# Kernel optimization log

Hardware: AMD Instinct MI355X
Metric: run time of the kernel (lower is better)

The kernel has to match this reference:

```python
import jax, jax.numpy as jnp
import numpy as np

B, L, D, DH = 4, 2048, 1024, 2048

def setup_inputs() -> dict:
    key = jax.random.key(0)
    ks = jax.random.split(key, 9)
    return {
        "x": jax.random.normal(ks[0], (B, L, D), jnp.float32),
        "W_in": jax.random.normal(ks[1], (DH, D), jnp.float32) / np.sqrt(D).astype(np.float32),
        "b_in": jnp.zeros((DH,), jnp.float32),
        "W_out": jax.random.normal(ks[2], (D, DH), jnp.float32) / np.sqrt(DH).astype(np.float32),
        "b_out": jnp.zeros((D,), jnp.float32),
        "phazor": jax.random.normal(ks[3], (DH, 2), jnp.float32),
        "phazor_init": jax.random.normal(ks[4], (DH, 2), jnp.float32),
        "last_conv_re": jax.random.normal(ks[5], (B, DH), jnp.float32),
        "last_conv_im": jax.random.normal(ks[6], (B, DH), jnp.float32),
    }

def reference(x, W_in, b_in, W_out, b_out, phazor, phazor_init, last_conv_re, last_conv_im):
    batch, length, _ = x.shape
    # linear_in, cast to float32 (already fp32 here)
    h = x @ W_in.T + b_in                                  # [B, L, DH]
    # view_as_complex of [DH, 2] params
    p = phazor[:, 0] + 1j * phazor[:, 1]                   # [DH]
    p0 = phazor_init[:, 0] + 1j * phazor_init[:, 1]        # [DH]
    pa = jnp.abs(p)
    p = p / pa * jnp.exp(-pa)                              # unit phase, exp(-|p|) magnitude
    # phazor_progression[t, c] = p[c] ** t
    prog = p[None, :] ** jnp.arange(length)[:, None]       # [L, DH] complex
    filt = prog * p0[None, :]                              # [L, DH]
    # FFT convolution with zero padding to 2L (linear convolution)
    ff = jnp.fft.fft(filt, n=2 * length, axis=0)           # [2L, DH]
    xf = jnp.fft.fft(h, n=2 * length, axis=1)              # [B, 2L, DH]
    conv = jnp.fft.ifft(ff[None] * xf, axis=1)[:, :length] # [B, L, DH]
    # add decayed contribution of past state (detached state)
    last = last_conv_re + 1j * last_conv_im                # [B, DH]
    conv_with_past = conv + last[:, None, :] * prog[None] * p[None, None, :]
    y = jax.nn.silu(conv_with_past.real)                   # back to real dtype
    return y @ W_out.T + b_out                             # [B, L, D]
```

## Files before the change

kernel.cpp:

```cpp
#include <hip/hip_runtime.h>
#include <math.h>

#define WS_B  4
#define WS_L  2048
#define WS_D  1024
#define WS_DH 2048
#define WS_M  (WS_B * WS_L)
#define NCH   128
#define CHUNK (WS_L / NCH)
#define CB    8

typedef __attribute__((ext_vector_type(4))) float     f32x4;
typedef _Float16 f16x8 __attribute__((ext_vector_type(8)));
typedef _Float16 f16x4 __attribute__((ext_vector_type(4)));

#define GLDS(gptr, lptr) \
    __builtin_amdgcn_global_load_lds( \
        (const __attribute__((address_space(1))) unsigned int*)(gptr), \
        (__attribute__((address_space(3))) unsigned int*)(lptr), 16, 0, 0)

__device__ inline void pack_tile(const float* __restrict__ src, _Float16* __restrict__ dst,
                                 int K, int rb, int kb, int tid, _Float16 (*sT)[136]) {
    const int K8 = K >> 3;
#pragma unroll
    for (int it = 0; it < 16; ++it) {
        int f    = it * 256 + tid;
        int row  = f >> 5;
        int col  = (f & 31) * 4;
        f32x4 v  = *(const f32x4*)(src + (size_t)(rb * 128 + row) * K + kb * 128 + col);
        f16x4 hv;
#pragma unroll
        for (int k = 0; k < 4; ++k) hv[k] = (_Float16)v[k];
        *(f16x4*)&sT[row][col] = hv;
    }
    __syncthreads();
#pragma unroll
    for (int it = 0; it < 8; ++it) {
        int c2 = it * 256 + tid;
        int r  = c2 & 127;
        int kq = c2 >> 7;
        f16x8 hv = *(const f16x8*)&sT[r][kq * 8];
        size_t chunk = ((size_t)rb * K8 + kb * 16 + kq) * 128 + r;
        *(f16x8*)(dst + chunk * 8) = hv;
    }
}

__global__ __launch_bounds__(256)
void pack_all(const float* __restrict__ x,     _Float16* __restrict__ xp,
              const float* __restrict__ W_in,  _Float16* __restrict__ w1p,
              const float* __restrict__ W_out, _Float16* __restrict__ w2p) {
    __shared__ alignas(16) _Float16 sT[128][136];
    const int tid = threadIdx.x;
    const int bid = blockIdx.x;
    if (bid < 512)      pack_tile(x,     xp,  WS_D,  bid >> 3,          bid & 7,          tid, sT);
    else if (bid < 640) pack_tile(W_in,  w1p, WS_D,  (bid - 512) >> 3,  (bid - 512) & 7,  tid, sT);
    else                pack_tile(W_out, w2p, WS_DH, (bid - 640) >> 4,  (bid - 640) & 15, tid, sT);
}

template<int K8, int LDC, int KQ, int MINB, typename OutT>
__global__ __launch_bounds__(256, MINB)
void gemm_f16_packed(const _Float16* __restrict__ A, const _Float16* __restrict__ B,
                     const float* __restrict__ bias, OutT* __restrict__ C)
{
    __shared__ alignas(16) _Float16 sA[2][KQ][128][8];
    __shared__ alignas(16) _Float16 sB[2][KQ][128][8];

    const int tid  = threadIdx.x;
    const int lane = tid & 63;
    const int wave = tid >> 6;
    const int wm   = (wave >> 1) * 64;
    const int wn   = (wave & 1) * 64;
    const int m15  = lane & 15;
    const int q    = lane >> 4;

    const int bm = blockIdx.x;
    const int bn = blockIdx.y;

    f32x4 acc[4][4] = {};

    auto stage = [&](int kc0, int buf) {
#pragma unroll
        for (int i = 0; i < KQ / 2; ++i) {
            int c   = i * 256 + tid;
            int row = c & 127;
            int kq  = c >> 7;
            size_t ac = ((size_t)(bm * K8 + kc0 + kq) * 128 + row) * 8;
            size_t bc = ((size_t)(bn * K8 + kc0 + kq) * 128 + row) * 8;
            GLDS(A + ac, &sA[buf][kq][row][0]);
            GLDS(B + bc, &sB[buf][kq][row][0]);
        }
    };

    auto compute = [&](int bufc) {
#pragma unroll
        for (int kk = 0; kk < KQ / 4; ++kk) {
            f16x8 af[4], bf[4];
#pragma unroll
            for (int i = 0; i < 4; ++i) {
                af[i] = *(const f16x8*)&sA[bufc][kk * 4 + q][wm + i * 16 + m15][0];
                bf[i] = *(const f16x8*)&sB[bufc][kk * 4 + q][wn + i * 16 + m15][0];
            }
#pragma unroll
            for (int i = 0; i < 4; ++i)
#pragma unroll
                for (int j = 0; j < 4; ++j)
                    acc[i][j] = __builtin_amdgcn_mfma_f32_16x16x32_f16(af[i], bf[j], acc[i][j], 0, 0, 0);
        }
    };

    stage(0, 0);
    stage(KQ, 1);

    int buf = 0;
    for (int kc0 = 0; kc0 + KQ < K8; kc0 += KQ, buf ^= 1) {
        asm volatile("s_waitcnt vmcnt(8)" ::: "memory");
        __builtin_amdgcn_sched_barrier(0);
        __builtin_amdgcn_s_barrier();

        compute(buf);

        __builtin_amdgcn_sched_barrier(0);
        __builtin_amdgcn_s_barrier();
        if (kc0 + 2 * KQ < K8) stage(kc0 + 2 * KQ, buf);
    }

    asm volatile("s_waitcnt vmcnt(0)" ::: "memory");
    __builtin_amdgcn_sched_barrier(0);
    __builtin_amdgcn_s_barrier();
    compute(buf);

    const int r4 = (lane >> 4) * 4;
#pragma unroll
    for (int j = 0; j < 4; ++j) {
        int col = bn * 128 + wn + j * 16 + m15;
        float bv = bias[col];
#pragma unroll
        for (int i = 0; i < 4; ++i) {
            int row0 = bm * 128 + wm + i * 16 + r4;
#pragma unroll
            for (int r = 0; r < 4; ++r)
                C[(size_t)(row0 + r) * LDC + col] = (OutT)(acc[i][j][r] + bv);
        }
    }
}

__device__ inline void compute_p(const float* __restrict__ phazor, int c, float& pre, float& pim) {
    float zr = phazor[2 * c], zi = phazor[2 * c + 1];
    float pa = sqrtf(zr * zr + zi * zi);
    float sc = expf(-pa) / pa;
    pre = zr * sc;
    pim = zi * sc;
}

__global__ void scan_local(const _Float16* __restrict__ h, const float* __restrict__ phazor,
                           const float* __restrict__ phazor_init, float* __restrict__ Uend) {
    int idx = blockIdx.x * blockDim.x + threadIdx.x;
    int cb   = idx & (WS_DH / CB - 1);
    int rest = idx >> 8;
    int j    = rest & (NCH - 1);
    int b    = rest >> 7;
    int c0   = cb * CB;
    float pre[CB], pim[CB], p0r[CB], p0i[CB], ur[CB] = {}, ui[CB] = {};
#pragma unroll
    for (int u = 0; u < CB; ++u) {
        compute_p(phazor, c0 + u, pre[u], pim[u]);
        p0r[u] = phazor_init[2 * (c0 + u)];
        p0i[u] = phazor_init[2 * (c0 + u) + 1];
    }
    const int row0 = b * WS_L + j * CHUNK;
    const _Float16* hp = h + (size_t)row0 * WS_DH + c0;
#pragma unroll
    for (int t = 0; t < CHUNK; ++t) {
        f16x8 v = *(const f16x8*)(hp + (size_t)t * WS_DH);
#pragma unroll
        for (int u = 0; u < CB; ++u) {
            float hv = (float)v[u];
            float nr = fmaf(pre[u], ur[u], fmaf(-pim[u], ui[u], p0r[u] * hv));
            float ni = fmaf(pre[u], ui[u], fmaf( pim[u], ur[u], p0i[u] * hv));
            ur[u] = nr; ui[u] = ni;
        }
    }
    float2* Ue = (float2*)Uend;
    size_t o = ((size_t)(b * NCH + j)) * WS_DH + c0;
#pragma unroll
    for (int u = 0; u < CB; ++u) { float2 w; w.x = ur[u]; w.y = ui[u]; Ue[o + u] = w; }
}

__global__ __launch_bounds__(256)
void scan_carry(const float* __restrict__ Uend, float* __restrict__ carry,
                const float* __restrict__ phazor,
                const float* __restrict__ last_re, const float* __restrict__ last_im) {
    __shared__ float2 T[16][NCH + 1];
    const int tid = threadIdx.x;
    const int blk = blockIdx.x;
    const int b   = blk >> 7;
    const int c0  = (blk & 127) * 16;

    const float2* Ue = (const float2*)Uend;
    float2* Ca = (float2*)carry;

    {
        int c_l = tid & 15, kq = tid >> 4;
#pragma unroll
        for (int pass = 0; pass < NCH / 16; ++pass) {
            int k = pass * 16 + kq;
            T[c_l][k] = Ue[(size_t)(b * NCH + k) * WS_DH + c0 + c_l];
        }
    }
    __syncthreads();

    const int j  = tid & 63;
    const int wv = tid >> 6;
#pragma unroll
    for (int pass = 0; pass < 4; ++pass) {
        int c_l = pass * 4 + wv;
        int c   = c0 + c_l;
        float pre, pim;
        compute_p(phazor, c, pre, pim);
        float qr = pre, qi = pim;
#pragma unroll
        for (int s = 0; s < 4; ++s) { float nr = qr*qr - qi*qi; qi = 2.f*qr*qi; qr = nr; }
        float q2r = qr*qr - qi*qi, q2i = 2.f*qr*qi;

        float2 L0 = T[c_l][2*j], L1 = T[c_l][2*j + 1];
        float lsr = fmaf(qr, L0.x, fmaf(-qi, L0.y, L1.x));
        float lsi = fmaf(qr, L0.y, fmaf( qi, L0.x, L1.y));
        float wr = 1.f, wi = 0.f, sr = q2r, si = q2i;
#pragma unroll
        for (int s = 0; s < 6; ++s) {
            if ((j >> s) & 1) { float nr = wr*sr - wi*si; wi = wr*si + wi*sr; wr = nr; }
            float n2 = sr*sr - si*si; si = 2.f*sr*si; sr = n2;
        }
        float xr = lsr, xi = lsi, ar = q2r, ai = q2i;
#pragma unroll
        for (int o = 1; o < 64; o <<= 1) {
            float rr = __shfl_up(xr, o);
            float ri = __shfl_up(xi, o);
            if (j >= o) {
                xr = fmaf(ar, rr, fmaf(-ai, ri, xr));
                xi = fmaf(ar, ri, fmaf( ai, rr, xi));
            }
            float n2 = ar*ar - ai*ai; ai = 2.f*ar*ai; ar = n2;
        }
        float tpr = __shfl_up(xr, 1), tpi = __shfl_up(xi, 1);
        if (j == 0) { tpr = 0.f; tpi = 0.f; }
        float Lre = last_re[b * WS_DH + c], Lim = last_im[b * WS_DH + c];
        float cer = fmaf(wr, Lre, fmaf(-wi, Lim, tpr));
        float cei = fmaf(wr, Lim, fmaf( wi, Lre, tpi));
        float cor = fmaf(qr, cer, fmaf(-qi, cei, L0.x));
        float coi = fmaf(qr, cei, fmaf( qi, cer, L0.y));
        T[c_l][2*j]     = make_float2(cer, cei);
        T[c_l][2*j + 1] = make_float2(cor, coi);
    }
    __syncthreads();

    {
        int c_l = tid & 15, kq = tid >> 4;
#pragma unroll
        for (int pass = 0; pass < NCH / 16; ++pass) {
            int k = pass * 16 + kq;
            Ca[(size_t)(b * NCH + k) * WS_DH + c0 + c_l] = T[c_l][k];
        }
    }
}

__global__ void scan_apply(const _Float16* __restrict__ h, const float* __restrict__ phazor,
                           const float* __restrict__ phazor_init, const float* __restrict__ carry,
                           _Float16* __restrict__ yh) {
    int idx = blockIdx.x * blockDim.x + threadIdx.x;
    int cb   = idx & (WS_DH / CB - 1);
    int rest = idx >> 8;
    int j    = rest & (NCH - 1);
    int b    = rest >> 7;
    int c0   = cb * CB;
    float pre[CB], pim[CB], p0r[CB], p0i[CB], ur[CB], ui[CB];
    const float2* Ca = (const float2*)carry;
    size_t co = ((size_t)(b * NCH + j)) * WS_DH + c0;
#pragma unroll
    for (int u = 0; u < CB; ++u) {
        compute_p(phazor, c0 + u, pre[u], pim[u]);
        p0r[u] = phazor_init[2 * (c0 + u)];
        p0i[u] = phazor_init[2 * (c0 + u) + 1];
        float2 w = Ca[co + u];
        ur[u] = w.x; ui[u] = w.y;
    }
    const int row0 = b * WS_L + j * CHUNK;
    const _Float16* hp = h + (size_t)row0 * WS_DH + c0;
#pragma unroll
    for (int t = 0; t < CHUNK; ++t) {
        f16x8 v = *(const f16x8*)(hp + (size_t)t * WS_DH);
        f16x8 yv;
#pragma unroll
        for (int u = 0; u < CB; ++u) {
            float hv = (float)v[u];
            float nr = fmaf(pre[u], ur[u], fmaf(-pim[u], ui[u], p0r[u] * hv));
            float ni = fmaf(pre[u], ui[u], fmaf( pim[u], ur[u], p0i[u] * hv));
            ur[u] = nr; ui[u] = ni;
            float z = nr;
            yv[u] = (_Float16)(z / (1.f + expf(-z)));
        }
        int row = row0 + t;
        size_t o = ((size_t)(row >> 7) * 256 + cb) * 128 + (row & 127);
        *(f16x8*)(yh + o * 8) = yv;
    }
}

extern "C" void kernel_launch(void* const* d_in, const int* in_sizes, int n_in,
                              void* d_out, int out_size, void* d_ws, size_t ws_size,
                              hipStream_t stream)
{
    const float* x       = (const float*)d_in[0];
    const float* W_in    = (const float*)d_in[1];
    const float* b_in    = (const float*)d_in[2];
    const float* W_out   = (const float*)d_in[3];
    const float* b_out   = (const float*)d_in[4];
    const float* phazor  = (const float*)d_in[5];
    const float* ph_init = (const float*)d_in[6];
    const float* last_re = (const float*)d_in[7];
    const float* last_im = (const float*)d_in[8];
    float* out = (float*)d_out;

    char* ws = (char*)d_ws;
    size_t off = 0;
    auto alloc = [&](size_t bytes) {
        char* p = ws + off;
        off += (bytes + 255) & ~(size_t)255;
        return p;
    };
    _Float16* h     = (_Float16*)alloc((size_t)WS_M * WS_DH * 2);
    _Float16* w2p   = (_Float16*)alloc((size_t)WS_D * WS_DH * 2);
    char*     alias0 = ws + off;
    _Float16* xp    = (_Float16*)alloc((size_t)WS_M * WS_D * 2);
    _Float16* w1p   = (_Float16*)alloc((size_t)WS_DH * WS_D * 2);
    float*    Uend  = (float*)alloc((size_t)WS_B * NCH * WS_DH * 2 * 4);
    alloc((size_t)4 * 1024 * 1024);
    float*    carry = (float*)alloc((size_t)WS_B * NCH * WS_DH * 2 * 4);
    _Float16* yhp   = (_Float16*)alias0;

    pack_all<<<dim3(768), dim3(256), 0, stream>>>(x, xp, W_in, w1p, W_out, w2p);

    {
        dim3 g(WS_M / 128, WS_DH / 128);
        gemm_f16_packed<WS_D / 8, WS_DH, 8, 2, _Float16><<<g, dim3(256), 0, stream>>>(xp, w1p, b_in, h);
    }

    {
        int total = WS_B * NCH * WS_DH / CB;
        scan_local<<<dim3(total / 256), dim3(256), 0, stream>>>(h, phazor, ph_init, Uend);
        scan_carry<<<dim3(WS_B * WS_DH / 16), dim3(256), 0, stream>>>(Uend, carry, phazor,
                                                                      last_re, last_im);
        scan_apply<<<dim3(total / 256), dim3(256), 0, stream>>>(h, phazor, ph_init, carry, yhp);
    }

    {
        dim3 g(WS_M / 128, WS_D / 128);
        gemm_f16_packed<WS_DH / 8, WS_D, 8, 2, float><<<g, dim3(256), 0, stream>>>(yhp, w2p, b_out, out);
    }
}
```

Baseline: 242.5 us.

## Replace packed k-chunk layout with row-major fp16 and XOR-swizzled LDS tiles

Drops the LDS-transposing pack kernel in favor of a simple elementwise fp32-to-fp16 conversion that keeps row-major layout. The GEMM now loads row-major tiles straight into LDS with an XOR swizzle on the 16-byte k-chunk index, which avoids bank conflicts on the MFMA fragment reads. scan_apply writes y in plain row-major order instead of the packed layout. Packing becomes cheaper and the scan output writes are contiguous per row, but each GEMM global load now spans row strides rather than fully contiguous 2KB chunks.

Measured after the change: 234.0 us. -3.5%, faster.

```diff
diff --git a/kernel.cpp b/kernel.cpp
--- a/kernel.cpp
+++ b/kernel.cpp
@@ -12,58 +12,41 @@
 
 typedef __attribute__((ext_vector_type(4))) float     f32x4;
 typedef _Float16 f16x8 __attribute__((ext_vector_type(8)));
-typedef _Float16 f16x4 __attribute__((ext_vector_type(4)));
 
 #define GLDS(gptr, lptr) \
     __builtin_amdgcn_global_load_lds( \
         (const __attribute__((address_space(1))) unsigned int*)(gptr), \
         (__attribute__((address_space(3))) unsigned int*)(lptr), 16, 0, 0)
 
-__device__ inline void pack_tile(const float* __restrict__ src, _Float16* __restrict__ dst,
-                                 int K, int rb, int kb, int tid, _Float16 (*sT)[136]) {
-    const int K8 = K >> 3;
-#pragma unroll
-    for (int it = 0; it < 16; ++it) {
-        int f    = it * 256 + tid;
-        int row  = f >> 5;
-        int col  = (f & 31) * 4;
-        f32x4 v  = *(const f32x4*)(src + (size_t)(rb * 128 + row) * K + kb * 128 + col);
-        f16x4 hv;
-#pragma unroll
-        for (int k = 0; k < 4; ++k) hv[k] = (_Float16)v[k];
-        *(f16x4*)&sT[row][col] = hv;
-    }
-    __syncthreads();
-#pragma unroll
-    for (int it = 0; it < 8; ++it) {
-        int c2 = it * 256 + tid;
-        int r  = c2 & 127;
-        int kq = c2 >> 7;
-        f16x8 hv = *(const f16x8*)&sT[r][kq * 8];
-        size_t chunk = ((size_t)rb * K8 + kb * 16 + kq) * 128 + r;
-        *(f16x8*)(dst + chunk * 8) = hv;
-    }
-}
 
 __global__ __launch_bounds__(256)
-void pack_all(const float* __restrict__ x,     _Float16* __restrict__ xp,
-              const float* __restrict__ W_in,  _Float16* __restrict__ w1p,
-              const float* __restrict__ W_out, _Float16* __restrict__ w2p) {
-    __shared__ alignas(16) _Float16 sT[128][136];
-    const int tid = threadIdx.x;
-    const int bid = blockIdx.x;
-    if (bid < 512)      pack_tile(x,     xp,  WS_D,  bid >> 3,          bid & 7,          tid, sT);
-    else if (bid < 640) pack_tile(W_in,  w1p, WS_D,  (bid - 512) >> 3,  (bid - 512) & 7,  tid, sT);
-    else                pack_tile(W_out, w2p, WS_DH, (bid - 640) >> 4,  (bid - 640) & 15, tid, sT);
-}
-
-template<int K8, int LDC, int KQ, int MINB, typename OutT>
+void convert_f16(const float* __restrict__ x,  _Float16* __restrict__ xh,
+                 const float* __restrict__ w1, _Float16* __restrict__ w1h,
+                 const float* __restrict__ w2, _Float16* __restrict__ w2h) {
+    const int n1 = WS_M * WS_D / 8;
+    const int n2 = WS_DH * WS_D / 8;
+    const int n3 = WS_D * WS_DH / 8;
+    int t = blockIdx.x * 256 + threadIdx.x;
+    const float* s; _Float16* d; int off;
+    if (t < n1)            { s = x;  d = xh;  off = t; }
+    else if (t < n1 + n2)  { s = w1; d = w1h; off = t - n1; }
+    else if (t < n1 + n2 + n3) { s = w2; d = w2h; off = t - n1 - n2; }
+    else return;
+    f32x4 v0 = *(const f32x4*)(s + (size_t)off * 8);
+    f32x4 v1 = *(const f32x4*)(s + (size_t)off * 8 + 4);
+    f16x8 h;
+#pragma unroll
+    for (int k = 0; k < 4; ++k) { h[k] = (_Float16)v0[k]; h[4 + k] = (_Float16)v1[k]; }
+    *(f16x8*)(d + (size_t)off * 8) = h;
+}
+
+template<int K, int LDC, int MINB, typename OutT>
 __global__ __launch_bounds__(256, MINB)
-void gemm_f16_packed(const _Float16* __restrict__ A, const _Float16* __restrict__ B,
-                     const float* __restrict__ bias, OutT* __restrict__ C)
+void gemm_f16(const _Float16* __restrict__ A, const _Float16* __restrict__ B,
+              const float* __restrict__ bias, OutT* __restrict__ C)
 {
-    __shared__ alignas(16) _Float16 sA[2][KQ][128][8];
-    __shared__ alignas(16) _Float16 sB[2][KQ][128][8];
+    __shared__ alignas(16) _Float16 sA[2][128 * 64];
+    __shared__ alignas(16) _Float16 sB[2][128 * 64];
 
     const int tid  = threadIdx.x;
     const int lane = tid & 63;
@@ -80,25 +63,26 @@
 
     auto stage = [&](int kc0, int buf) {
 #pragma unroll
-        for (int i = 0; i < KQ / 2; ++i) {
+        for (int i = 0; i < 4; ++i) {
             int c   = i * 256 + tid;
-            int row = c & 127;
-            int kq  = c >> 7;
-            size_t ac = ((size_t)(bm * K8 + kc0 + kq) * 128 + row) * 8;
-            size_t bc = ((size_t)(bn * K8 + kc0 + kq) * 128 + row) * 8;
-            GLDS(A + ac, &sA[buf][kq][row][0]);
-            GLDS(B + bc, &sB[buf][kq][row][0]);
+            int row = c >> 3;
+            int kqs = (c & 7) ^ (row & 7);
+            GLDS(A + (size_t)(bm * 128 + row) * K + kc0 + kqs * 8, &sA[buf][c * 8]);
+            GLDS(B + (size_t)(bn * 128 + row) * K + kc0 + kqs * 8, &sB[buf][c * 8]);
         }
     };
 
     auto compute = [&](int bufc) {
 #pragma unroll
-        for (int kk = 0; kk < KQ / 4; ++kk) {
+        for (int kk = 0; kk < 2; ++kk) {
             f16x8 af[4], bf[4];
+            int kq = kk * 4 + q;
 #pragma unroll
             for (int i = 0; i < 4; ++i) {
-                af[i] = *(const f16x8*)&sA[bufc][kk * 4 + q][wm + i * 16 + m15][0];
-                bf[i] = *(const f16x8*)&sB[bufc][kk * 4 + q][wn + i * 16 + m15][0];
+                int ra = wm + i * 16 + m15;
+                int rb = wn + i * 16 + m15;
+                af[i] = *(const f16x8*)&sA[bufc][ra * 64 + ((kq ^ (ra & 7)) << 3)];
+                bf[i] = *(const f16x8*)&sB[bufc][rb * 64 + ((kq ^ (rb & 7)) << 3)];
             }
 #pragma unroll
             for (int i = 0; i < 4; ++i)
@@ -109,10 +93,11 @@
     };
 
     stage(0, 0);
-    stage(KQ, 1);
+    stage(64, 1);
 
     int buf = 0;
-    for (int kc0 = 0; kc0 + KQ < K8; kc0 += KQ, buf ^= 1) {
+    int kc0 = 0;
+    for (; kc0 + 64 < K; kc0 += 64, buf ^= 1) {
         asm volatile("s_waitcnt vmcnt(8)" ::: "memory");
         __builtin_amdgcn_sched_barrier(0);
         __builtin_amdgcn_s_barrier();
@@ -121,7 +106,7 @@
 
         __builtin_amdgcn_sched_barrier(0);
         __builtin_amdgcn_s_barrier();
-        if (kc0 + 2 * KQ < K8) stage(kc0 + 2 * KQ, buf);
+        if (kc0 + 128 < K) stage(kc0 + 128, buf);
     }
 
     asm volatile("s_waitcnt vmcnt(0)" ::: "memory");
@@ -286,6 +271,7 @@
     }
     const int row0 = b * WS_L + j * CHUNK;
     const _Float16* hp = h + (size_t)row0 * WS_DH + c0;
+    _Float16* yp = yh + (size_t)row0 * WS_DH + c0;
 #pragma unroll
     for (int t = 0; t < CHUNK; ++t) {
         f16x8 v = *(const f16x8*)(hp + (size_t)t * WS_DH);
@@ -299,9 +285,7 @@
             float z = nr;
             yv[u] = (_Float16)(z / (1.f + expf(-z)));
         }
-        int row = row0 + t;
-        size_t o = ((size_t)(row >> 7) * 256 + cb) * 128 + (row & 127);
-        *(f16x8*)(yh + o * 8) = yv;
+        *(f16x8*)(yp + (size_t)t * WS_DH) = yv;
     }
 }
 
@@ -328,20 +312,23 @@
         return p;
     };
     _Float16* h     = (_Float16*)alloc((size_t)WS_M * WS_DH * 2);
-    _Float16* w2p   = (_Float16*)alloc((size_t)WS_D * WS_DH * 2);
+    _Float16* w2h   = (_Float16*)alloc((size_t)WS_D * WS_DH * 2);
     char*     alias0 = ws + off;
-    _Float16* xp    = (_Float16*)alloc((size_t)WS_M * WS_D * 2);
-    _Float16* w1p   = (_Float16*)alloc((size_t)WS_DH * WS_D * 2);
+    _Float16* xh    = (_Float16*)alloc((size_t)WS_M * WS_D * 2);
+    _Float16* w1h   = (_Float16*)alloc((size_t)WS_DH * WS_D * 2);
     float*    Uend  = (float*)alloc((size_t)WS_B * NCH * WS_DH * 2 * 4);
     alloc((size_t)4 * 1024 * 1024);
     float*    carry = (float*)alloc((size_t)WS_B * NCH * WS_DH * 2 * 4);
-    _Float16* yhp   = (_Float16*)alias0;
-
-    pack_all<<<dim3(768), dim3(256), 0, stream>>>(x, xp, W_in, w1p, W_out, w2p);
+    _Float16* yh    = (_Float16*)alias0;
+
+    {
+        int n = (WS_M * WS_D + WS_DH * WS_D + WS_D * WS_DH) / 8;
+        convert_f16<<<dim3((n + 255) / 256), dim3(256), 0, stream>>>(x, xh, W_in, w1h, W_out, w2h);
+    }
 
     {
         dim3 g(WS_M / 128, WS_DH / 128);
-        gemm_f16_packed<WS_D / 8, WS_DH, 8, 2, _Float16><<<g, dim3(256), 0, stream>>>(xp, w1p, b_in, h);
+        gemm_f16<WS_D, WS_DH, 2, _Float16><<<g, dim3(512 / 2), 0, stream>>>(xh, w1h, b_in, h);
     }
 
     {
@@ -349,11 +336,11 @@
         scan_local<<<dim3(total / 256), dim3(256), 0, stream>>>(h, phazor, ph_init, Uend);
         scan_carry<<<dim3(WS_B * WS_DH / 16), dim3(256), 0, stream>>>(Uend, carry, phazor,
                                                                       last_re, last_im);
-        scan_apply<<<dim3(total / 256), dim3(256), 0, stream>>>(h, phazor, ph_init, carry, yhp);
+        scan_apply<<<dim3(total / 256), dim3(256), 0, stream>>>(h, phazor, ph_init, carry, yh);
     }
 
     {
         dim3 g(WS_M / 128, WS_D / 128);
-        gemm_f16_packed<WS_DH / 8, WS_D, 8, 2, float><<<g, dim3(256), 0, stream>>>(yhp, w2p, b_out, out);
-    }
-}
+        gemm_f16<WS_DH, WS_D, 2, float><<<g, dim3(256), 0, stream>>>(yh, w2h, b_out, out);
+    }
+}
```
